# Optimization experiments

Measured on AMD Instinct MI355X. Metric: run time of the kernel, lower is better.

## Reference

```python
import jax, jax.numpy as jnp
import numpy as np

NUM_EMBEDDINGS = 1024
EMBED_DIM = 64
COMMITMENT_COST = 0.25
N_TOKENS = 131072


def setup_inputs() -> dict:
    key = jax.random.key(0)
    kx, kw = jax.random.split(key)
    x = jax.random.normal(kx, (N_TOKENS, EMBED_DIM), dtype=jnp.float32)
    # nn.Embedding weight, init normal(0, 1/num_embeddings)
    weight = jax.random.normal(kw, (NUM_EMBEDDINGS, EMBED_DIM), dtype=jnp.float32) * (1.0 / NUM_EMBEDDINGS)
    return {"x": x, "weight": weight}


def reference(x, weight):
    x_norm = jnp.sum(x * x, axis=1, keepdims=True)            # [N, 1]
    e_norm = jnp.sum(weight * weight, axis=1)                 # [K]
    distances = x_norm + e_norm - 2.0 * jnp.matmul(x, weight.T)
    embed_inds = jnp.argmin(distances, axis=1)                # [N] int
    x_quantized = jnp.take(weight, embed_inds, axis=0)        # [N, D]

    # Eval path (self.training == False): no EMA updates.
    codebook_loss = jnp.mean((jax.lax.stop_gradient(x_quantized) - x) ** 2)
    commitment_loss = jnp.mean((x_quantized - jax.lax.stop_gradient(x)) ** 2) * COMMITMENT_COST
    loss = codebook_loss + commitment_loss
    return x_quantized, loss, embed_inds
```

## Files before the change

kernel.cpp:

```cpp
#include <hip/hip_runtime.h>


#define N_TOK   131072
#define DIM     64
#define KCODES  1024
#define MARGIN  3e-5f
#define LOSS_POS ((size_t)8388608)
#define EN_OFF_F 98304
#define CNT_OFF  99328
#define WL_OFF   99332
#define WL_CAP   16384
#define WT_OFF   131072
#define SP_OFF   196608
#define RP_OFF   197632

typedef __attribute__((ext_vector_type(8))) short  short8;
typedef __attribute__((ext_vector_type(4))) float  float4v;

__device__ __forceinline__ unsigned bf16rne(float f) {
    unsigned u = __float_as_uint(f);
    return (u + 0x7FFFu + ((u >> 16) & 1u)) >> 16;
}
__device__ __forceinline__ float bf16tof(unsigned h) { return __uint_as_float(h << 16); }

__global__ __launch_bounds__(256) void k_prep(const float* __restrict__ w,
                                              float* __restrict__ wsf) {
    if (blockIdx.x == 0 && threadIdx.x == 0) ((int*)wsf)[CNT_OFF] = 0;
    if (blockIdx.x < 96) {
        const int g    = blockIdx.x * 256 + threadIdx.x;
        const int lane = g & 63;
        const int fs   = g >> 6;
        const int c = fs / 12, r = fs % 12, nt = r / 6, ks = r % 6;
        const int j    = c * 32 + nt * 16 + (lane & 15);
        const int quad = lane >> 4;
        const int kk   = ks * 32 + quad * 8;
        const bool hi  = (kk < 128);
        const int k0   = hi ? (kk & 63) : (kk - 128);
        const float4* src = (const float4*)(w + (size_t)j * DIM + k0);
        float4 v0 = src[0], v1 = src[1];
        float f[8] = {-2.0f * v0.x, -2.0f * v0.y, -2.0f * v0.z, -2.0f * v0.w,
                      -2.0f * v1.x, -2.0f * v1.y, -2.0f * v1.z, -2.0f * v1.w};
        unsigned o[4];
#pragma unroll
        for (int p = 0; p < 4; ++p) {
            unsigned h0 = bf16rne(f[2 * p]), h1 = bf16rne(f[2 * p + 1]);
            if (hi) o[p] = h0 | (h1 << 16);
            else {
                unsigned l0 = bf16rne(f[2 * p]     - bf16tof(h0));
                unsigned l1 = bf16rne(f[2 * p + 1] - bf16tof(h1));
                o[p] = l0 | (l1 << 16);
            }
        }
        *(uint4*)((unsigned*)wsf + (size_t)g * 4) = make_uint4(o[0], o[1], o[2], o[3]);
    } else if (blockIdx.x < 100) {
        const int row = (blockIdx.x - 96) * 256 + threadIdx.x;
        const float* wr = w + (size_t)row * DIM;
        double en = 0.0;
#pragma unroll 8
        for (int k = 0; k < DIM; ++k) { double v = wr[k]; en += v * v; }
        wsf[EN_OFF_F + row] = (float)en;
    } else {
        const int g  = (blockIdx.x - 100) * 256 + threadIdx.x;
        const int ob = g * 16;
        float* wT = wsf + WT_OFF;
#pragma unroll
        for (int m = 0; m < 16; ++m) {
            const int o = ob + m;
            const int j = o & 1023, k = o >> 10;
            wT[o] = w[(size_t)j * DIM + k];
        }
    }
}

__global__ __launch_bounds__(256, 4) void k_screen(
    const float* __restrict__ x, const float* __restrict__ w,
    float* __restrict__ wsf, float* __restrict__ out,
    float* __restrict__ idxf, int* __restrict__ wsi)
{
    __shared__ __align__(16) unsigned char smem[28672];
    unsigned* smemU = (unsigned*)smem;
    const float* en_s = (const float*)(smem + 24576);

    const int tid  = threadIdx.x;
    const int lane = tid & 63;
    const int wv   = tid >> 6;
    const int col  = lane & 15;
    const int quad = (lane >> 4) & 3;
    const int tokBase = blockIdx.x * 128;

    __builtin_amdgcn_global_load_lds(
        (const __attribute__((address_space(1))) void*)
            ((const unsigned char*)(wsf + EN_OFF_F) + tid * 16),
        (__attribute__((address_space(3))) void*)(smem + 24576 + tid * 16),
        16, 0, 0);

    short8 afrag[2][6];
    for (int pass = 0; pass < 2; ++pass) {
        const int row = tid >> 2, seg = tid & 3;
        const float4* xr = (const float4*)(x + (size_t)(tokBase + pass * 64 + row) * DIM + seg * 16);
        unsigned* rb = smemU + row * 96 + seg * 8;
#pragma unroll
        for (int q = 0; q < 4; ++q) {
            float4 v = xr[q];
            unsigned hx = bf16rne(v.x), hy = bf16rne(v.y);
            unsigned hz = bf16rne(v.z), hw = bf16rne(v.w);
            unsigned h01 = hx | (hy << 16), h23 = hz | (hw << 16);
            unsigned l01 = bf16rne(v.x - bf16tof(hx)) | (bf16rne(v.y - bf16tof(hy)) << 16);
            unsigned l23 = bf16rne(v.z - bf16tof(hz)) | (bf16rne(v.w - bf16tof(hw)) << 16);
            rb[2 * q] = h01;      rb[2 * q + 1] = h23;
            rb[32 + 2 * q] = l01; rb[32 + 2 * q + 1] = l23;
            rb[64 + 2 * q] = h01; rb[64 + 2 * q + 1] = h23;
        }
        __syncthreads();
        if ((wv >> 1) == pass) {
#pragma unroll
            for (int mt = 0; mt < 2; ++mt)
#pragma unroll
                for (int ks = 0; ks < 6; ++ks)
                    afrag[mt][ks] = *(const short8*)(smem
                        + ((wv & 1) * 32 + mt * 16 + col) * 384 + ks * 64 + quad * 16);
        }
        __syncthreads();
    }

    float m1[8], m2[8];
#pragma unroll
    for (int i = 0; i < 8; ++i) { m1[i] = 3.4e38f; m2[i] = 3.4e38f; }

    float4v acc[2][2];
    {
        const float e0 = en_s[col], e1 = en_s[16 + col];
#pragma unroll
        for (int mt = 0; mt < 2; ++mt) {
            acc[mt][0] = (float4v){e0, e0, e0, e0};
            acc[mt][1] = (float4v){e1, e1, e1, e1};
        }
    }

    const unsigned char* wext = (const unsigned char*)wsf;

    {
        const unsigned char* gsrc = wext + tid * 16;
        unsigned char*       ldst = smem + tid * 16;
#pragma unroll
        for (int it = 0; it < 3; ++it)
            __builtin_amdgcn_global_load_lds(
                (const __attribute__((address_space(1))) void*)(gsrc + it * 4096),
                (__attribute__((address_space(3))) void*)(ldst + it * 4096),
                16, 0, 0);
    }
    __syncthreads();

    for (int c = 0; c < 32; ++c) {
        const int cur = c & 1;
        if (c < 31) {
            const unsigned char* gsrc = wext + (c + 1) * 12288 + tid * 16;
            unsigned char*       ldst = smem + (cur ^ 1) * 12288 + tid * 16;
#pragma unroll
            for (int it = 0; it < 3; ++it)
                __builtin_amdgcn_global_load_lds(
                    (const __attribute__((address_space(1))) void*)(gsrc + it * 4096),
                    (__attribute__((address_space(3))) void*)(ldst + it * 4096),
                    16, 0, 0);
        }

        const unsigned char* bbase = smem + cur * 12288 + (size_t)lane * 16;
#pragma unroll
        for (int ks = 0; ks < 6; ++ks) {
            short8 b0 = *(const short8*)(bbase + (ks)     * 1024);
            short8 b1 = *(const short8*)(bbase + (6 + ks) * 1024);
            acc[0][0] = __builtin_amdgcn_mfma_f32_16x16x32_bf16(afrag[0][ks], b0, acc[0][0], 0, 0, 0);
            acc[1][0] = __builtin_amdgcn_mfma_f32_16x16x32_bf16(afrag[1][ks], b0, acc[1][0], 0, 0, 0);
            acc[0][1] = __builtin_amdgcn_mfma_f32_16x16x32_bf16(afrag[0][ks], b1, acc[0][1], 0, 0, 0);
            acc[1][1] = __builtin_amdgcn_mfma_f32_16x16x32_bf16(afrag[1][ks], b1, acc[1][1], 0, 0, 0);
        }

        {
            float ecn0 = 0.0f, ecn1 = 0.0f;
            if (c < 31) {
                ecn0 = en_s[(c + 1) * 32 + col];
                ecn1 = en_s[(c + 1) * 32 + 16 + col];
            }
#pragma unroll
            for (int nt = 0; nt < 2; ++nt) {
                const unsigned jg = (unsigned)(c * 32 + nt * 16 + col);
                const float ecn = nt ? ecn1 : ecn0;
#pragma unroll
                for (int mt = 0; mt < 2; ++mt)
#pragma unroll
                    for (int r = 0; r < 4; ++r) {
                        const int t = mt * 4 + r;
                        float p = __uint_as_float((__float_as_uint(acc[mt][nt][r]) & 0xFFFFFC00u) | jg);
                        m2[t] = __builtin_amdgcn_fmed3f(m1[t], m2[t], p);
                        m1[t] = fminf(m1[t], p);
                        acc[mt][nt][r] = ecn;
                    }
            }
        }
        __syncthreads();
    }

#pragma unroll
    for (int m = 1; m <= 8; m <<= 1) {
#pragma unroll
        for (int t = 0; t < 8; ++t) {
            float o1 = __shfl_xor(m1[t], m, 64);
            float o2 = __shfl_xor(m2[t], m, 64);
            m2[t] = fminf(fminf(m2[t], o2), fmaxf(m1[t], o1));
            m1[t] = fminf(m1[t], o1);
        }
    }

    float* idxl_s = (float*)smem;
    double* rr    = (double*)(smem + 1024);
    if (col == 0) {
#pragma unroll
        for (int t = 0; t < 8; ++t) {
            const int mt = t >> 2, r = t & 3;
            const int tokLocal = wv * 32 + mt * 16 + quad * 4 + r;
            const int tok = tokBase + tokLocal;
            const int id  = (int)(__float_as_uint(m1[t]) & 1023u);
            const bool flagged = (m2[t] - m1[t] < MARGIN);
            idxf[tok] = (float)id;
            idxl_s[tokLocal] = flagged ? -(float)(id + 1) : (float)id;
            if (flagged) {
                int p = atomicAdd(wsi + CNT_OFF, 1);
                if (p < WL_CAP) wsi[WL_OFF + p] = tok;
            }
        }
    }
    __syncthreads();

    {
        const float4* x4 = (const float4*)x;
        const float4* w4 = (const float4*)w;
        float4*       o4 = (float4*)out;
        double lacc = 0.0;
#pragma unroll 4
        for (int kk = 0; kk < 8; ++kk) {
            const int li = tid + kk * 256;
            const float fid = idxl_s[li >> 4];
            if (fid >= 0.0f) {
                const int id = (int)fid;
                const size_t gi = (size_t)tokBase * 16 + li;
                float4 xv  = x4[gi];
                float4 wvv = w4[(size_t)id * 16 + (li & 15)];
                o4[gi] = wvv;
                float dx = xv.x - wvv.x, dy = xv.y - wvv.y;
                float dz = xv.z - wvv.z, dw = xv.w - wvv.w;
                lacc += (double)dx * dx + (double)dy * dy + (double)dz * dz + (double)dw * dw;
            }
        }
        rr[tid] = lacc;
        __syncthreads();
        for (int off = 128; off > 0; off >>= 1) {
            if (tid < off) rr[tid] += rr[tid + off];
            __syncthreads();
        }
        if (tid == 0) wsf[SP_OFF + blockIdx.x] = (float)rr[0];
    }
}

__global__ __launch_bounds__(256) void k_resolve(
    const float* __restrict__ x, const float* __restrict__ w,
    float* __restrict__ wsf, float* __restrict__ idxf,
    float* __restrict__ out, const int* __restrict__ wsi)
{
    __shared__ float xs[4][DIM];
    const int tid  = threadIdx.x;
    const int lane = tid & 63;
    const int wv   = tid >> 6;
    const int g    = blockIdx.x * 4 + wv;
    int n = wsi[CNT_OFF];
    if (n > WL_CAP) n = WL_CAP;
    const float4* wT4 = (const float4*)(wsf + WT_OFF);
    const float4* en4 = (const float4*)(wsf + EN_OFF_F);
    double lacc = 0.0;

    for (int i = g; i < n; i += 1024) {
        const int ft = wsi[WL_OFF + i];
        xs[wv][lane] = x[(size_t)ft * DIM + lane];

        double xnd = 0.0;
        for (int k = 0; k < DIM; ++k) { double xv = (double)xs[wv][k]; xnd += xv * xv; }
        const float xn = (float)xnd;

        float dbest = 3.4e38f; int jbest = 0;
        for (int jj = 0; jj < 4; ++jj) {
            const int idx = lane + jj * 64;
            float ca0 = 0.f, ca1 = 0.f, ca2 = 0.f, ca3 = 0.f;
#pragma unroll 16
            for (int k = 0; k < DIM; ++k) {
                float4 wv4 = wT4[k * 256 + idx];
                const float xk = xs[wv][k];
                ca0 = __fmaf_rn(xk, wv4.x, ca0);
                ca1 = __fmaf_rn(xk, wv4.y, ca1);
                ca2 = __fmaf_rn(xk, wv4.z, ca2);
                ca3 = __fmaf_rn(xk, wv4.w, ca3);
            }
            const float4 ev = en4[idx];
            const int jb = idx * 4;
            float d0 = __fsub_rn(__fadd_rn(xn, ev.x), __fmul_rn(2.0f, ca0));
            float d1 = __fsub_rn(__fadd_rn(xn, ev.y), __fmul_rn(2.0f, ca1));
            float d2 = __fsub_rn(__fadd_rn(xn, ev.z), __fmul_rn(2.0f, ca2));
            float d3 = __fsub_rn(__fadd_rn(xn, ev.w), __fmul_rn(2.0f, ca3));
            if (d0 < dbest) { dbest = d0; jbest = jb;     }
            if (d1 < dbest) { dbest = d1; jbest = jb + 1; }
            if (d2 < dbest) { dbest = d2; jbest = jb + 2; }
            if (d3 < dbest) { dbest = d3; jbest = jb + 3; }
        }
#pragma unroll
        for (int m = 1; m < 64; m <<= 1) {
            float od = __shfl_xor(dbest, m, 64);
            int   oj = __shfl_xor(jbest, m, 64);
            if (od < dbest || (od == dbest && oj < jbest)) { dbest = od; jbest = oj; }
        }
        if (lane == 0) idxf[ft] = (float)jbest;

        if (lane < 16) {
            const float4* x4 = (const float4*)x;
            const float4* w4 = (const float4*)w;
            float4*       o4 = (float4*)out;
            float4 wvv = w4[(size_t)jbest * 16 + lane];
            float4 xv  = x4[(size_t)ft * 16 + lane];
            o4[(size_t)ft * 16 + lane] = wvv;
            float dx = xv.x - wvv.x, dy = xv.y - wvv.y;
            float dz = xv.z - wvv.z, dw = xv.w - wvv.w;
            lacc += (double)dx * dx + (double)dy * dy + (double)dz * dz + (double)dw * dw;
        }
    }

#pragma unroll
    for (int m = 1; m < 64; m <<= 1) lacc += __shfl_xor(lacc, m, 64);
    if (lane == 0) wsf[RP_OFF + g] = (float)lacc;
}

__global__ __launch_bounds__(256) void k_loss(const float* __restrict__ wsf,
                                              float* __restrict__ out) {
    __shared__ double r[256];
    const int t = threadIdx.x;
    double s = 0.0;
#pragma unroll
    for (int i = 0; i < 4; ++i) s += (double)wsf[SP_OFF + t + i * 256];
#pragma unroll
    for (int i = 0; i < 4; ++i) s += (double)wsf[RP_OFF + t + i * 256];
    r[t] = s;
    __syncthreads();
    for (int off = 128; off > 0; off >>= 1) {
        if (t < off) r[t] += r[t + off];
        __syncthreads();
    }
    if (t == 0) out[LOSS_POS] = (float)(r[0] * 1.25 / 8388608.0);
}

extern "C" void kernel_launch(void* const* d_in, const int* in_sizes, int n_in,
                              void* d_out, int out_size, void* d_ws, size_t ws_size,
                              hipStream_t stream) {
    const float* x = (const float*)d_in[0];
    const float* w = (const float*)d_in[1];
    float* out = (float*)d_out;
    float* idxf = out + LOSS_POS + 1;
    float* wsf  = (float*)d_ws;
    int*   wsi  = (int*)d_ws;

    k_prep<<<116, 256, 0, stream>>>(w, wsf);
    k_screen<<<N_TOK / 128, 256, 0, stream>>>(x, w, wsf, out, idxf, wsi);
    k_resolve<<<256, 256, 0, stream>>>(x, w, wsf, idxf, out, wsi);
    k_loss<<<1, 256, 0, stream>>>(wsf, out);
}
```

Before: 183.0 us.

## Resolve ambiguous tokens with one block per token and drop duplicate LDS writes

The exact-fp32 resolve kernel now gives each flagged token a full 256-thread block, one thread per four codes, instead of one wavefront per token looping over four code chunks. The per-wave argmin shuffle becomes an LDS tree reduction with barriers, and the loss partials shrink to one value per block. The main kernel also stops writing a third copy of the high bf16 half to LDS and reuses the already loaded A fragments instead. The resolve path adds many __syncthreads per token, and its grid size must now match the 256 partial slots that k_loss reads.

```diff
diff --git a/kernel.cpp b/kernel.cpp
--- a/kernel.cpp
+++ b/kernel.cpp
@@ -109,16 +109,18 @@
             unsigned l23 = bf16rne(v.z - bf16tof(hz)) | (bf16rne(v.w - bf16tof(hw)) << 16);
             rb[2 * q] = h01;      rb[2 * q + 1] = h23;
             rb[32 + 2 * q] = l01; rb[32 + 2 * q + 1] = l23;
-            rb[64 + 2 * q] = h01; rb[64 + 2 * q + 1] = h23;
         }
         __syncthreads();
         if ((wv >> 1) == pass) {
 #pragma unroll
-            for (int mt = 0; mt < 2; ++mt)
-#pragma unroll
-                for (int ks = 0; ks < 6; ++ks)
+            for (int mt = 0; mt < 2; ++mt) {
+#pragma unroll
+                for (int ks = 0; ks < 4; ++ks)
                     afrag[mt][ks] = *(const short8*)(smem
                         + ((wv & 1) * 32 + mt * 16 + col) * 384 + ks * 64 + quad * 16);
+                afrag[mt][4] = afrag[mt][0];
+                afrag[mt][5] = afrag[mt][1];
+            }
         }
         __syncthreads();
     }
@@ -266,73 +268,81 @@
     float* __restrict__ wsf, float* __restrict__ idxf,
     float* __restrict__ out, const int* __restrict__ wsi)
 {
-    __shared__ float xs[4][DIM];
-    const int tid  = threadIdx.x;
-    const int lane = tid & 63;
-    const int wv   = tid >> 6;
-    const int g    = blockIdx.x * 4 + wv;
+    __shared__ float  xf[DIM];
+    __shared__ float  rd[256];
+    __shared__ int    rj[256];
+    __shared__ double rl[256];
+    const int tid = threadIdx.x;
     int n = wsi[CNT_OFF];
     if (n > WL_CAP) n = WL_CAP;
     const float4* wT4 = (const float4*)(wsf + WT_OFF);
     const float4* en4 = (const float4*)(wsf + EN_OFF_F);
     double lacc = 0.0;
 
-    for (int i = g; i < n; i += 1024) {
+    for (int i = blockIdx.x; i < n; i += gridDim.x) {
         const int ft = wsi[WL_OFF + i];
-        xs[wv][lane] = x[(size_t)ft * DIM + lane];
+        if (tid < DIM) xf[tid] = x[(size_t)ft * DIM + tid];
+        __syncthreads();
 
         double xnd = 0.0;
-        for (int k = 0; k < DIM; ++k) { double xv = (double)xs[wv][k]; xnd += xv * xv; }
+        for (int k = 0; k < DIM; ++k) { double xv = (double)xf[k]; xnd += xv * xv; }
         const float xn = (float)xnd;
 
-        float dbest = 3.4e38f; int jbest = 0;
-        for (int jj = 0; jj < 4; ++jj) {
-            const int idx = lane + jj * 64;
-            float ca0 = 0.f, ca1 = 0.f, ca2 = 0.f, ca3 = 0.f;
-#pragma unroll 16
-            for (int k = 0; k < DIM; ++k) {
-                float4 wv4 = wT4[k * 256 + idx];
-                const float xk = xs[wv][k];
-                ca0 = __fmaf_rn(xk, wv4.x, ca0);
-                ca1 = __fmaf_rn(xk, wv4.y, ca1);
-                ca2 = __fmaf_rn(xk, wv4.z, ca2);
-                ca3 = __fmaf_rn(xk, wv4.w, ca3);
-            }
-            const float4 ev = en4[idx];
-            const int jb = idx * 4;
-            float d0 = __fsub_rn(__fadd_rn(xn, ev.x), __fmul_rn(2.0f, ca0));
-            float d1 = __fsub_rn(__fadd_rn(xn, ev.y), __fmul_rn(2.0f, ca1));
-            float d2 = __fsub_rn(__fadd_rn(xn, ev.z), __fmul_rn(2.0f, ca2));
-            float d3 = __fsub_rn(__fadd_rn(xn, ev.w), __fmul_rn(2.0f, ca3));
-            if (d0 < dbest) { dbest = d0; jbest = jb;     }
-            if (d1 < dbest) { dbest = d1; jbest = jb + 1; }
-            if (d2 < dbest) { dbest = d2; jbest = jb + 2; }
-            if (d3 < dbest) { dbest = d3; jbest = jb + 3; }
-        }
-#pragma unroll
-        for (int m = 1; m < 64; m <<= 1) {
-            float od = __shfl_xor(dbest, m, 64);
-            int   oj = __shfl_xor(jbest, m, 64);
-            if (od < dbest || (od == dbest && oj < jbest)) { dbest = od; jbest = oj; }
-        }
-        if (lane == 0) idxf[ft] = (float)jbest;
-
-        if (lane < 16) {
+        float ca0 = 0.f, ca1 = 0.f, ca2 = 0.f, ca3 = 0.f;
+#pragma unroll 8
+        for (int k = 0; k < DIM; ++k) {
+            float4 wv4 = wT4[k * 256 + tid];
+            const float xk = xf[k];
+            ca0 = __fmaf_rn(xk, wv4.x, ca0);
+            ca1 = __fmaf_rn(xk, wv4.y, ca1);
+            ca2 = __fmaf_rn(xk, wv4.z, ca2);
+            ca3 = __fmaf_rn(xk, wv4.w, ca3);
+        }
+        const float4 ev = en4[tid];
+        const int jb = tid * 4;
+        float d0 = __fsub_rn(__fadd_rn(xn, ev.x), __fmul_rn(2.0f, ca0));
+        float d1 = __fsub_rn(__fadd_rn(xn, ev.y), __fmul_rn(2.0f, ca1));
+        float d2 = __fsub_rn(__fadd_rn(xn, ev.z), __fmul_rn(2.0f, ca2));
+        float d3 = __fsub_rn(__fadd_rn(xn, ev.w), __fmul_rn(2.0f, ca3));
+        float dbest = d0; int jbest = jb;
+        if (d1 < dbest) { dbest = d1; jbest = jb + 1; }
+        if (d2 < dbest) { dbest = d2; jbest = jb + 2; }
+        if (d3 < dbest) { dbest = d3; jbest = jb + 3; }
+        rd[tid] = dbest; rj[tid] = jbest;
+        __syncthreads();
+        for (int off = 128; off > 0; off >>= 1) {
+            if (tid < off) {
+                float od = rd[tid + off]; int oj = rj[tid + off];
+                if (od < rd[tid] || (od == rd[tid] && oj < rj[tid])) {
+                    rd[tid] = od; rj[tid] = oj;
+                }
+            }
+            __syncthreads();
+        }
+        const int jwin = rj[0];
+        if (tid == 0) idxf[ft] = (float)jwin;
+
+        if (tid < 16) {
             const float4* x4 = (const float4*)x;
             const float4* w4 = (const float4*)w;
             float4*       o4 = (float4*)out;
-            float4 wvv = w4[(size_t)jbest * 16 + lane];
-            float4 xv  = x4[(size_t)ft * 16 + lane];
-            o4[(size_t)ft * 16 + lane] = wvv;
+            float4 wvv = w4[(size_t)jwin * 16 + tid];
+            float4 xv  = x4[(size_t)ft * 16 + tid];
+            o4[(size_t)ft * 16 + tid] = wvv;
             float dx = xv.x - wvv.x, dy = xv.y - wvv.y;
             float dz = xv.z - wvv.z, dw = xv.w - wvv.w;
             lacc += (double)dx * dx + (double)dy * dy + (double)dz * dz + (double)dw * dw;
         }
-    }
-
-#pragma unroll
-    for (int m = 1; m < 64; m <<= 1) lacc += __shfl_xor(lacc, m, 64);
-    if (lane == 0) wsf[RP_OFF + g] = (float)lacc;
+        __syncthreads();
+    }
+
+    rl[tid] = lacc;
+    __syncthreads();
+    for (int off = 128; off > 0; off >>= 1) {
+        if (tid < off) rl[tid] += rl[tid + off];
+        __syncthreads();
+    }
+    if (tid == 0) wsf[RP_OFF + blockIdx.x] = (float)rl[0];
 }
 
 __global__ __launch_bounds__(256) void k_loss(const float* __restrict__ wsf,
@@ -342,8 +352,7 @@
     double s = 0.0;
 #pragma unroll
     for (int i = 0; i < 4; ++i) s += (double)wsf[SP_OFF + t + i * 256];
-#pragma unroll
-    for (int i = 0; i < 4; ++i) s += (double)wsf[RP_OFF + t + i * 256];
+    s += (double)wsf[RP_OFF + t];
     r[t] = s;
     __syncthreads();
     for (int off = 128; off > 0; off >>= 1) {
```

Result: faster. 165.0 us (median of 2 runs) (-9.9%).
